# Kernel optimization log

Measured on AMD Instinct MI355X. Metric: run time of the kernel, lower is better.

Reference implementation:

```python
import jax, jax.numpy as jnp
import numpy as np

_LOG_2PI = float(np.log(2.0 * np.pi))
N = 4096
N_VARS = 128
N_SOURCES = 8
_EPS = 1e-6


def setup_inputs() -> dict:
    key = jax.random.key(0)
    ks = jax.random.split(key, 6)
    data = jax.random.normal(ks[0], (N, N_VARS), dtype=jnp.float32)
    sources = jax.random.randint(ks[1], (N,), 0, N_SOURCES, dtype=jnp.int32)
    miss_mask = jax.random.bernoulli(ks[2], 0.3, (N, N_VARS))
    # Strictly lower-triangular DAG weights, small spectral norm so I - W is well conditioned
    W_eff = jnp.tril(jax.random.normal(ks[3], (N_VARS, N_VARS), dtype=jnp.float32) * 0.05, k=-1)
    log_sigma2 = jnp.zeros((N_SOURCES, N_VARS), dtype=jnp.float32)
    mu = jnp.zeros((N_VARS,), dtype=jnp.float32)
    sample_weights = jax.random.uniform(ks[4], (N,), dtype=jnp.float32)
    return {"data": data, "W_eff": W_eff, "log_sigma2": log_sigma2, "mu": mu,
            "sample_weights": sample_weights, "sources": sources, "miss_mask": miss_mask}


def reference(data, W_eff, log_sigma2, mu, sample_weights, sources, miss_mask):
    # Gaussian log-likelihood over observed entries only, per sample.
    # Original torch code loops over unique (source, missingness-pattern) groups and
    # does a Cholesky of the observed sub-covariance Sigma_oo + eps*I.  We compute the
    # mathematically identical quantity fully batched via the masked-covariance trick:
    #   Sigma_tilde = M (Sigma + eps I) M + diag(1 - obs)
    # whose logdet equals logdet(Sigma_oo + eps I_oo) and whose quadratic form on the
    # zero-filled centred data equals x_o^T (Sigma_oo + eps I)^{-1} x_o.
    D = data.shape[1]
    I = jnp.eye(D, dtype=data.dtype)
    T = jnp.linalg.solve(I - W_eff, I)                       # [D, D]
    sigma2 = jnp.maximum(jnp.exp(log_sigma2), _EPS)          # [S, D]
    # Sigma_s = T^T diag(sigma2_s) T for every source
    Sigma = jnp.einsum('ij,si,ik->sjk', T, sigma2, T)        # [S, D, D]

    obs = (~miss_mask).astype(data.dtype)                    # [N, D]
    xc = (data - mu[None, :]) * obs                          # centred, zero at missing

    Sig_i = Sigma[sources] + _EPS * I                        # [N, D, D]
    M = obs[:, :, None] * obs[:, None, :]                    # [N, D, D] obs outer obs
    Sig_t = Sig_i * M + I * (1.0 - obs)[:, None, :]          # identity on missing coords

    L = jnp.linalg.cholesky(Sig_t)                           # [N, D, D]
    z = jax.scipy.linalg.solve_triangular(L, xc[:, :, None], lower=True)[:, :, 0]
    quad = jnp.sum(z * z, axis=1)                            # [N]
    logdet = 2.0 * jnp.sum(jnp.log(jnp.diagonal(L, axis1=1, axis2=2)), axis=1)
    d_obs = jnp.sum(obs, axis=1)                             # [N]
    ll = -0.5 * (quad + logdet + d_obs * _LOG_2PI)           # [N]
    return jnp.sum(ll * sample_weights)
```

## Files before the change

### kernel.cpp

```cpp
#include <hip/hip_runtime.h>
#include <math.h>

#define DD 128
#define NSRC 8
#define EMAX 32
#define MFAST 62
#define LOG_2PI 1.83787706640934548356f
#define LN2F 0.69314718055994531f
#define EPSF 1e-6f

__device__ inline int tri_row_of(int e) {
    float f = sqrtf(8.f * (float)e + 1.f);
    int r = (int)((f - 1.f) * 0.5f);
    if ((r + 1) * (r + 2) / 2 <= e) ++r;
    else if (r * (r + 1) / 2 > e) --r;
    return r;
}

__global__ __launch_bounds__(128) void k_precompute(
    const float* __restrict__ W, const float* __restrict__ ls2,
    const unsigned int* __restrict__ mw, int n_words,
    float* __restrict__ Q, float* __restrict__ ldS,
    int* __restrict__ flagarr, float* __restrict__ partial,
    int* __restrict__ ovf_cnt)
{
    __shared__ float Bs[DD][DD + 1];
    __shared__ float r[4][DD + 1];
    __shared__ float sinv[DD];
    __shared__ float part2[2];
    __shared__ int fsh[2];
    const int tid = threadIdx.x;
    const int s   = blockIdx.x >> 5;
    const int i0  = (blockIdx.x & 31) * 4;

    if (blockIdx.x == 0) {
        if (tid < 64)  partial[tid] = 0.f;
        if (tid == 64) *ovf_cnt = 0;
    }

    int gid = (blockIdx.x * 128 + tid) * 4;
    int f = 0;
    #pragma unroll
    for (int t = 0; t < 4; ++t) {
        int idx = gid + t;
        if (idx < n_words) {
            unsigned int v = mw[idx];
            if (v > 1u) f |= 1;
            if (v == 0x3F800000u) f |= 2;
        }
    }
    unsigned long long bA = __ballot(f & 1);
    unsigned long long bB = __ballot(f & 2);
    if ((tid & 63) == 0) fsh[tid >> 6] = (bA ? 1 : 0) | (bB ? 2 : 0);

    for (int idx = tid; idx < DD * DD; idx += 128) {
        int row = idx >> 7, col = idx & 127;
        Bs[row][col] = (row == col ? 1.f : 0.f) - W[idx];
    }
    sinv[tid] = 1.f / fmaxf(expf(ls2[s * DD + tid]), EPSF);
    __syncthreads();
    if (tid == 0) flagarr[blockIdx.x] = fsh[0] | fsh[1];
    for (int a = 0; a < 4; ++a)
        r[a][tid] = Bs[i0 + a][tid] * sinv[tid];
    __syncthreads();

    const int j = tid;
    float acc0 = 0.f, acc1 = 0.f, acc2 = 0.f, acc3 = 0.f;
    #pragma unroll 4
    for (int d = 0; d < DD; ++d) {
        float bj = Bs[j][d];
        acc0 += r[0][d] * bj;
        acc1 += r[1][d] * bj;
        acc2 += r[2][d] * bj;
        acc3 += r[3][d] * bj;
    }
    size_t base = ((size_t)s * DD + i0) * DD + j;
    Q[base         ] = acc0;
    Q[base +     DD] = acc1;
    Q[base + 2 * DD] = acc2;
    Q[base + 3 * DD] = acc3;

    if (i0 == 0) {
        float v = logf(fmaxf(expf(ls2[s * DD + tid]), EPSF));
        for (int o = 32; o; o >>= 1) v += __shfl_down(v, o, 64);
        if ((tid & 63) == 0) part2[tid >> 6] = v;
        __syncthreads();
        if (tid == 0) ldS[s] = part2[0] + part2[1];
    }
}

__global__ __launch_bounds__(64) void k_fast(
    const float* __restrict__ data, const float* __restrict__ mu,
    const float* __restrict__ wgt, const int* __restrict__ src,
    const void* __restrict__ miss, const int* __restrict__ flagarr,
    const float* __restrict__ Q, const float* __restrict__ ldS,
    float* __restrict__ partial, int* __restrict__ ovf_cnt,
    int* __restrict__ ovf_list)
{
    __shared__ float xsh[DD];
    __shared__ float ysh[DD];
    __shared__ int   midx[64];
    __shared__ float csc[2][64];
    __shared__ float tri[(MFAST + 1) * (MFAST + 2) / 2];

    const int i = blockIdx.x, lane = threadIdx.x;
    const int s = src[i];
    const float* Qs = Q + (size_t)s * DD * DD;
    const size_t base = (size_t)i * DD;
    const int j0 = 2 * lane, j1 = 2 * lane + 1;

    int fl = 0;
    #pragma unroll
    for (int t = 0; t < 4; ++t) fl |= flagarr[lane + 64 * t];
    unsigned long long fb1 = __ballot(fl & 1);
    unsigned long long fb2 = __ballot(fl & 2);
    const int f = (fb1 ? 1 : 0) | (fb2 ? 2 : 0);

    bool mmE, mmO;
    if (f & 2) {
        const float* M = (const float*)miss;
        mmE = M[base + j0] != 0.f;  mmO = M[base + j1] != 0.f;
    } else if (f & 1) {
        const unsigned char* M = (const unsigned char*)miss;
        mmE = M[base + j0] != 0;    mmO = M[base + j1] != 0;
    } else {
        const int* M = (const int*)miss;
        mmE = M[base + j0] != 0;    mmO = M[base + j1] != 0;
    }

    unsigned long long bE = __ballot(mmE), bO = __ballot(mmO);
    const int m = __popcll(bE) + __popcll(bO);
    if (m > MFAST) {
        if (lane == 0) { int pos = atomicAdd(ovf_cnt, 1); ovf_list[pos] = i; }
        return;
    }
    unsigned long long lt = (1ull << lane) - 1ull;
    if (mmE) midx[__popcll(bE & lt)] = j0;
    if (mmO) midx[__popcll(bE) + __popcll(bO & lt)] = j1;

    float x0 = mmE ? 0.f : (data[base + j0] - mu[j0]);
    float x1 = mmO ? 0.f : (data[base + j1] - mu[j1]);
    xsh[j0] = x0;
    xsh[j1] = x1;
    __syncthreads();

    float y0 = 0.f, y1 = 0.f, z0 = 0.f, z1 = 0.f;
    #pragma unroll 8
    for (int k = 0; k < DD; k += 2) {
        float xk0 = xsh[k], xk1 = xsh[k + 1];
        float2 qa = *(const float2*)(Qs + (size_t)k * DD + j0);
        float2 qb = *(const float2*)(Qs + (size_t)(k + 1) * DD + j0);
        y0 += xk0 * qa.x;  y1 += xk0 * qa.y;
        z0 += xk1 * qb.x;  z1 += xk1 * qb.y;
    }
    y0 += z0;  y1 += z1;
    ysh[j0] = y0;
    ysh[j1] = y1;
    float p = x0 * y0 + x1 * y1;
    for (int o = 32; o; o >>= 1) p += __shfl_down(p, o, 64);
    __syncthreads();

    const int mjc = midx[lane];
    for (int ir = 0; ir < m; ++ir) {
        int row = midx[ir];
        if (lane <= ir)
            tri[((ir * (ir + 1)) >> 1) + lane] = Qs[(size_t)row * DD + mjc];
    }
    const int offm = (m * (m + 1)) >> 1;
    if (lane < m)   tri[offm + lane] = ysh[mjc];
    if (lane == 0)  tri[offm + m] = 0.f;
    __syncthreads();

    const int cntT = ((m + 1) * (m + 2)) >> 1;
    unsigned key[EMAX];
    float    val[EMAX];
    #pragma unroll
    for (int t = 0; t < EMAX; ++t) {
        key[t] = 0u; val[t] = 0.f;
        int e = lane + (t << 6);
        if (e < cntT) {
            int q  = tri_row_of(e);
            int jc = m - q;
            int ir = jc + (e - ((q * (q + 1)) >> 1));
            float v = tri[((ir * (ir + 1)) >> 1) + jc];
            key[t] = ((unsigned)jc << 8) | (unsigned)ir;
            val[t] = v;
            if (jc == 0) csc[0][ir] = v;
        }
    }
    __syncthreads();

    float logacc = 0.f;
    #pragma unroll 1
    for (int k = 0; k < m; ++k) {
        const int pb = k & 1;
        float dk = csc[pb][k];
        float invd = __builtin_amdgcn_rcpf(dk);
        logacc += __log2f(dk);
        const unsigned boundA = (unsigned)(k + 1) << 8;
        const unsigned boundB = (unsigned)(k + 2) << 8;
        #pragma unroll
        for (int t = 0; t < EMAX; ++t) {
            bool alive = (key[t] >= boundA);
            if (!__any(alive)) break;
            if (alive) {
                int ir = (int)(key[t] & 255u);
                int jc = (int)(key[t] >> 8);
                float ci = csc[pb][ir];
                float cj = csc[pb][jc];
                val[t] -= ci * cj * invd;
                if (key[t] < boundB) csc[pb ^ 1][ir] = val[t];
            }
        }
        __syncthreads();
    }

    if (lane == 0) {
        float ll = -0.5f * ((p + val[0]) + logacc * LN2F + ldS[s]
                            + (float)(DD - m) * LOG_2PI);
        atomicAdd(&partial[i & 63], ll * wgt[i]);
    }
}

__global__ __launch_bounds__(128) void k_tail(
    const float* __restrict__ data, const float* __restrict__ mu,
    const float* __restrict__ wgt, const int* __restrict__ src,
    const void* __restrict__ miss, const int* __restrict__ flagarr,
    const float* __restrict__ Q, const float* __restrict__ ldS,
    float* __restrict__ partial, const int* __restrict__ ovf_cnt,
    const int* __restrict__ ovf_list, float* __restrict__ out)
{
    __shared__ __align__(16) float xsh[DD];
    __shared__ float ysh[DD];
    __shared__ int   midx[DD];
    __shared__ float cscv[DD + 1];
    __shared__ float tri[(DD + 1) * (DD + 2) / 2];
    __shared__ float bc[2];
    __shared__ float red[2];
    __shared__ int   sh_m;
    __shared__ int   sh_f;

    const int tid = threadIdx.x;
    if (tid == 0) sh_f = 0;
    __syncthreads();
    {
        int fl = flagarr[tid] | flagarr[tid + 128];
        if (fl) atomicOr(&sh_f, fl);
    }
    __syncthreads();
    const int f = sh_f;

    const int novf = *ovf_cnt;
    for (int j = 0; j < novf; ++j) {
        const int i = ovf_list[j];
        if (tid == 0) sh_m = 0;
        __syncthreads();

        const int s = src[i];
        const float* Qs = Q + (size_t)s * DD * DD;
        const size_t g = (size_t)i * DD + tid;
        bool mm;
        if (f & 2)      mm = ((const float*)miss)[g] != 0.f;
        else if (f & 1) mm = ((const unsigned char*)miss)[g] != 0;
        else            mm = ((const int*)miss)[g] != 0;

        float xv = mm ? 0.f : (data[g] - mu[tid]);
        xsh[tid] = xv;
        if (mm) { int pos = atomicAdd(&sh_m, 1); midx[pos] = tid; }
        __syncthreads();
        const int m = sh_m;

        const float4* qrow = (const float4*)(Qs + (size_t)tid * DD);
        const float4* x4   = (const float4*)xsh;
        float acc = 0.f;
        #pragma unroll 8
        for (int d = 0; d < DD / 4; ++d) {
            float4 q = qrow[d], xx = x4[d];
            acc += q.x * xx.x + q.y * xx.y + q.z * xx.z + q.w * xx.w;
        }
        ysh[tid] = acc;
        float pp = xv * acc;
        for (int o = 32; o; o >>= 1) pp += __shfl_down(pp, o, 64);
        if ((tid & 63) == 0) red[tid >> 6] = pp;
        __syncthreads();

        const int cntA = (m * (m + 1)) >> 1;
        for (int e = tid; e < cntA; e += 128) {
            int a = tri_row_of(e);
            int b = e - ((a * (a + 1)) >> 1);
            tri[e] = Qs[(size_t)midx[a] * DD + midx[b]];
        }
        for (int b = tid; b < m; b += 128) tri[cntA + b] = ysh[midx[b]];
        if (tid == 0) tri[cntA + m] = 0.f;
        __syncthreads();

        float logacc = 0.f;
        if (m > 0) {
            if (tid == 0) {
                float d0 = tri[0];
                bc[1] = d0;
                float sq = sqrtf(d0);
                bc[0] = 1.f / sq;
                tri[0] = sq;
            }
            __syncthreads();
            for (int k = 0; k < m; ++k) {
                float inv = bc[0];
                if (tid == 0) logacc += logf(bc[1]);
                for (int ii = k + 1 + tid; ii <= m; ii += 128) {
                    int off = (ii * (ii + 1)) >> 1;
                    float v = tri[off + k] * inv;
                    tri[off + k] = v;
                    cscv[ii] = v;
                }
                __syncthreads();
                int qn  = m - k;
                int cnt = (qn * (qn + 1)) >> 1;
                for (int e = tid; e < cnt; e += 128) {
                    int ri = tri_row_of(e);
                    int rj = e - ((ri * (ri + 1)) >> 1);
                    int ii = k + 1 + ri, jj = k + 1 + rj;
                    int off = (ii * (ii + 1)) >> 1;
                    float v = tri[off + jj] - cscv[ii] * cscv[jj];
                    if (ii == jj && jj == k + 1 && k + 1 < m) {
                        bc[1] = v;
                        float sq = sqrtf(v);
                        bc[0] = 1.f / sq;
                        tri[off + jj] = sq;
                    } else {
                        tri[off + jj] = v;
                    }
                }
                __syncthreads();
            }
        }

        if (tid == 0) {
            float quad2 = (m > 0) ? -tri[cntA + m] : 0.f;
            float quad1 = red[0] + red[1];
            float ll = -0.5f * ((quad1 - quad2) + logacc + ldS[s]
                                + (float)(DD - m) * LOG_2PI);
            atomicAdd(&partial[i & 63], ll * wgt[i]);
        }
        __syncthreads();
    }

    __syncthreads();
    if (tid < 64) {
        float v = partial[tid];
        for (int o = 32; o; o >>= 1) v += __shfl_down(v, o, 64);
        if (tid == 0) out[0] = v;
    }
}

extern "C" void kernel_launch(void* const* d_in, const int* in_sizes, int n_in,
                              void* d_out, int out_size, void* d_ws, size_t ws_size,
                              hipStream_t stream)
{
    const float* data = (const float*)d_in[0];
    const float* W    = (const float*)d_in[1];
    const float* ls2  = (const float*)d_in[2];
    const float* mu   = (const float*)d_in[3];
    const float* wgt  = (const float*)d_in[4];
    const int*   src  = (const int*)d_in[5];
    const void*  miss = (const void*)d_in[6];
    float* out = (float*)d_out;

    float* Q        = (float*)d_ws;
    float* ldS      = Q + (size_t)NSRC * DD * DD;
    float* partial  = ldS + NSRC;
    int*   flagarr  = (int*)(partial + 64);
    int*   ovf_cnt  = flagarr + 256;
    int*   ovf_list = ovf_cnt + 1;

    const int n       = in_sizes[0] / DD;
    const int n_words = (n * DD) / 4;

    hipLaunchKernelGGL(k_precompute, dim3(NSRC * 32), dim3(128), 0, stream,
                       W, ls2, (const unsigned int*)miss, n_words,
                       Q, ldS, flagarr, partial, ovf_cnt);
    hipLaunchKernelGGL(k_fast, dim3(n), dim3(64), 0, stream,
                       data, mu, wgt, src, miss, flagarr, Q, ldS,
                       partial, ovf_cnt, ovf_list);
    hipLaunchKernelGGL(k_tail, dim3(1), dim3(128), 0, stream,
                       data, mu, wgt, src, miss, flagarr, Q, ldS,
                       partial, ovf_cnt, ovf_list, out);
}
```

Before: 157.0 us.

## Block the in-register LDL elimination two pivots per step in fast kernel

Restructures the per-sample Gaussian elimination loop in the fast path so each iteration eliminates two pivots at once (a 2x2 block update), storing the two active columns as a float2 buffer. This halves the number of barrier-separated iterations and the passes over the register-held triangle entries, cutting sync and loop overhead. Each update now does more arithmetic, and there is a tail step for odd sizes. The reordered floating-point operations may change rounding slightly.

```diff
diff --git a/kernel.cpp b/kernel.cpp
--- a/kernel.cpp
+++ b/kernel.cpp
@@ -100,7 +100,7 @@
     __shared__ float xsh[DD];
     __shared__ float ysh[DD];
     __shared__ int   midx[64];
-    __shared__ float csc[2][64];
+    __shared__ float2 csc2[2][64];
     __shared__ float tri[(MFAST + 1) * (MFAST + 2) / 2];
 
     const int i = blockIdx.x, lane = threadIdx.x;
@@ -185,20 +185,26 @@
             float v = tri[((ir * (ir + 1)) >> 1) + jc];
             key[t] = ((unsigned)jc << 8) | (unsigned)ir;
             val[t] = v;
-            if (jc == 0) csc[0][ir] = v;
+            if (jc == 0)      csc2[0][ir].x = v;
+            else if (jc == 1) csc2[0][ir].y = v;
         }
     }
     __syncthreads();
 
     float logacc = 0.f;
+    int k = 0, sb = 0;
     #pragma unroll 1
-    for (int k = 0; k < m; ++k) {
-        const int pb = k & 1;
-        float dk = csc[pb][k];
-        float invd = __builtin_amdgcn_rcpf(dk);
-        logacc += __log2f(dk);
-        const unsigned boundA = (unsigned)(k + 1) << 8;
-        const unsigned boundB = (unsigned)(k + 2) << 8;
+    while (k + 1 < m) {
+        float2 pk  = csc2[sb][k];
+        float2 pk1 = csc2[sb][k + 1];
+        float invd0 = __builtin_amdgcn_rcpf(pk.x);
+        float s01   = pk1.x * invd0;
+        float d1    = pk1.y - pk1.x * s01;
+        float invd1 = __builtin_amdgcn_rcpf(d1);
+        logacc += __log2f(pk.x) + __log2f(d1);
+        const unsigned boundA = (unsigned)(k + 2) << 8;
+        const unsigned boundX = (unsigned)(k + 3) << 8;
+        const unsigned boundY = (unsigned)(k + 4) << 8;
         #pragma unroll
         for (int t = 0; t < EMAX; ++t) {
             bool alive = (key[t] >= boundA);
@@ -206,13 +212,25 @@
             if (alive) {
                 int ir = (int)(key[t] & 255u);
                 int jc = (int)(key[t] >> 8);
-                float ci = csc[pb][ir];
-                float cj = csc[pb][jc];
-                val[t] -= ci * cj * invd;
-                if (key[t] < boundB) csc[pb ^ 1][ir] = val[t];
+                float2 ci = csc2[sb][ir];
+                float2 cj = csc2[sb][jc];
+                float bi = ci.y - ci.x * s01;
+                float bj = cj.y - cj.x * s01;
+                val[t] -= ci.x * cj.x * invd0 + bi * bj * invd1;
+                if (key[t] < boundX)      csc2[sb ^ 1][ir].x = val[t];
+                else if (key[t] < boundY) csc2[sb ^ 1][ir].y = val[t];
             }
         }
         __syncthreads();
+        sb ^= 1;
+        k += 2;
+    }
+    if (k < m) {
+        float2 pk = csc2[sb][k];
+        float invd0 = __builtin_amdgcn_rcpf(pk.x);
+        logacc += __log2f(pk.x);
+        float2 cm = csc2[sb][m];
+        if (lane == 0) val[0] -= cm.x * cm.x * invd0;
     }
 
     if (lane == 0) {
```

Result: slower. 162.4 us (+3.4%).
